# Kernel tuning notes

Measured on AMD Instinct MI355X. Metric: run time of the kernel, lower is better.

Reference implementation:

```python
import jax, jax.numpy as jnp
import numpy as np

N_HEAD, D_K, D_V, D_MODEL, D_O = 8, 64, 64, 512, 512
B, S = 2, 4096

def setup_inputs() -> dict:
    key = jax.random.key(0)
    ks = jax.random.split(key, 11)
    s = 1.0 / np.sqrt(D_MODEL)
    so = 1.0 / np.sqrt(N_HEAD * D_V)
    return {
        'q': jax.random.normal(ks[0], (B, S, D_MODEL), jnp.float32),
        'k': jax.random.normal(ks[1], (B, S, D_MODEL), jnp.float32),
        'v': jax.random.normal(ks[2], (B, S, D_MODEL), jnp.float32),
        'Wq': jax.random.uniform(ks[3], (D_MODEL, N_HEAD * D_K), jnp.float32, -s, s),
        'bq': jax.random.uniform(ks[4], (N_HEAD * D_K,), jnp.float32, -s, s),
        'Wk': jax.random.uniform(ks[5], (D_MODEL, N_HEAD * D_K), jnp.float32, -s, s),
        'bk': jax.random.uniform(ks[6], (N_HEAD * D_K,), jnp.float32, -s, s),
        'Wv': jax.random.uniform(ks[7], (D_MODEL, N_HEAD * D_V), jnp.float32, -s, s),
        'bv': jax.random.uniform(ks[8], (N_HEAD * D_V,), jnp.float32, -s, s),
        'Wo': jax.random.uniform(ks[9], (N_HEAD * D_V, D_O), jnp.float32, -so, so),
        'bo': jax.random.uniform(ks[10], (D_O,), jnp.float32, -so, so),
    }

def reference(q, k, v, Wq, bq, Wk, bk, Wv, bv, Wo, bo):
    b, nq, _ = q.shape
    nk = k.shape[1]
    scale = jnp.asarray(np.power(D_K, 0.5), q.dtype)
    # project and split heads: [b, s, h, d]
    qh = (q @ Wq + bq).reshape(b, nq, N_HEAD, D_K)
    kh = (k @ Wk + bk).reshape(b, nk, N_HEAD, D_K)
    vh = (v @ Wv + bv).reshape(b, nk, N_HEAD, D_V)
    # scaled dot-product attention (full score matrix, as in original)
    scores = jnp.einsum('bqhd,bkhd->bhqk', qh, kh) / scale
    attn = jax.nn.softmax(scores, axis=-1)
    out = jnp.einsum('bhqk,bkhd->bqhd', attn, vh)
    # concat heads (head-major over d_v, matching the original view) and output proj
    out = out.reshape(b, nq, N_HEAD * D_V)
    return out @ Wo + bo
```

## Files before the change

### kernel.cpp

```cpp
#include <hip/hip_runtime.h>
#include <hip/hip_bf16.h>

#define NHEAD 8
#define DK_ 64
#define DM_ 512
#define S_LEN 4096
#define NTOK 8192

typedef __bf16 bf16x8 __attribute__((ext_vector_type(8)));
typedef float f32x4 __attribute__((ext_vector_type(4)));

__device__ __forceinline__ unsigned short f2bf(float f) {
    union { float f; unsigned u; } x; x.f = f;
    unsigned u = x.u;
    u += 0x7FFFu + ((u >> 16) & 1u);
    return (unsigned short)(u >> 16);
}

#if __has_builtin(__builtin_amdgcn_cvt_pk_bf16_f32)
__device__ __forceinline__ unsigned int pkbf(float a, float b) {
    auto r = __builtin_amdgcn_cvt_pk_bf16_f32(a, b);
    unsigned int u; __builtin_memcpy(&u, &r, 4); return u;
}
#else
__device__ __forceinline__ unsigned int pkbf(float a, float b) {
    return (unsigned)f2bf(a) | ((unsigned)f2bf(b) << 16);
}
#endif

#if __has_builtin(__builtin_amdgcn_exp2f)
#define EXP2F(x) __builtin_amdgcn_exp2f(x)
#else
#define EXP2F(x) exp2f(x)
#endif

#define GLOAD_LDS16(gptr, ldsbase) \
    __builtin_amdgcn_global_load_lds((const __attribute__((address_space(1))) unsigned int*)(gptr), \
                                     (__attribute__((address_space(3))) unsigned int*)(ldsbase), 16, 0, 0)

__global__ __launch_bounds__(256) void wtrans(const float* __restrict__ Wq, const float* __restrict__ Wk,
                                              const float* __restrict__ Wv, const float* __restrict__ Wo,
                                              unsigned short* __restrict__ Wt) {
    int z = blockIdx.z;
    const float* W = (z == 0) ? Wq : (z == 1) ? Wk : (z == 2) ? Wv : Wo;
    unsigned short* out = Wt + (size_t)z * DM_ * DM_;
    __shared__ float t[64][65];
    int bn = blockIdx.x * 64, bk = blockIdx.y * 64;
    int tid = threadIdx.x;
    int r0 = tid >> 4, c4 = (tid & 15) * 4;
#pragma unroll
    for (int i = 0; i < 4; i++) {
        int r = r0 + i * 16;
        float4 v = *(const float4*)&W[(size_t)(bk + r) * DM_ + bn + c4];
        t[r][c4] = v.x; t[r][c4 + 1] = v.y; t[r][c4 + 2] = v.z; t[r][c4 + 3] = v.w;
    }
    __syncthreads();
    int n0 = tid >> 4, k4 = (tid & 15) * 4;
#pragma unroll
    for (int i = 0; i < 4; i++) {
        int n = n0 + i * 16;
        ushort4 o;
        o.x = f2bf(t[k4 + 0][n]); o.y = f2bf(t[k4 + 1][n]);
        o.z = f2bf(t[k4 + 2][n]); o.w = f2bf(t[k4 + 3][n]);
        *(ushort4*)&out[(size_t)(bn + n) * DM_ + bk + k4] = o;
    }
}

__global__ __launch_bounds__(256, 3) void qkv_proj(const float* __restrict__ xq, const float* __restrict__ xk,
                                                   const float* __restrict__ xv, const unsigned short* __restrict__ Wt,
                                                   const float* __restrict__ bq, const float* __restrict__ bk,
                                                   const float* __restrict__ bv,
                                                   unsigned short* __restrict__ Qh, unsigned short* __restrict__ Kh,
                                                   unsigned short* __restrict__ VhT) {
    int z = blockIdx.z;
    const float* X = (z == 0) ? xq : (z == 1) ? xk : xv;
    const unsigned short* W = Wt + (size_t)z * DM_ * DM_;
    const float* bias = (z == 0) ? bq : (z == 1) ? bk : bv;
    unsigned short* out = (z == 0) ? Qh : (z == 1) ? Kh : VhT;
    float scale = (z == 0) ? 0.125f * 1.44269504f : 1.0f;

    __shared__ unsigned short As[128 * 40];
    __shared__ unsigned short Bs[128 * 40];
    int tid = threadIdx.x;
    int n0 = blockIdx.x * 128, m0 = blockIdx.y * 128;
    int w = tid >> 6, lane = tid & 63;
    int ln = lane & 15, qd = lane >> 4;
    int mb = (w >> 1) * 64, nb = (w & 1) * 64;

    f32x4 acc[4][4];
#pragma unroll
    for (int i = 0; i < 4; i++)
#pragma unroll
        for (int j = 0; j < 4; j++) { f32x4 zz = {0.f, 0.f, 0.f, 0.f}; acc[i][j] = zz; }

    for (int kk = 0; kk < DM_; kk += 32) {
        __syncthreads();
#pragma unroll
        for (int i = 0; i < 4; i++) {
            int idx = i * 256 + tid;
            int row = idx >> 3, k4 = (idx & 7) * 4;
            float4 v = *(const float4*)&X[(size_t)(m0 + row) * DM_ + kk + k4];
            uint2 o; o.x = pkbf(v.x, v.y); o.y = pkbf(v.z, v.w);
            *(uint2*)&As[row * 40 + k4] = o;
        }
#pragma unroll
        for (int i = 0; i < 2; i++) {
            int idx = i * 256 + tid;
            int row = idx >> 2, k8 = (idx & 3) * 8;
            uint4 v = *(const uint4*)&W[(size_t)(n0 + row) * DM_ + kk + k8];
            *(uint4*)&Bs[row * 40 + k8] = v;
        }
        __syncthreads();
        bf16x8 af[4], bf[4];
#pragma unroll
        for (int mt = 0; mt < 4; mt++) af[mt] = *(const bf16x8*)&As[(mb + mt * 16 + ln) * 40 + qd * 8];
#pragma unroll
        for (int nt = 0; nt < 4; nt++) bf[nt] = *(const bf16x8*)&Bs[(nb + nt * 16 + ln) * 40 + qd * 8];
#pragma unroll
        for (int mt = 0; mt < 4; mt++)
#pragma unroll
            for (int nt = 0; nt < 4; nt++)
                acc[mt][nt] = __builtin_amdgcn_mfma_f32_16x16x32_bf16(af[mt], bf[nt], acc[mt][nt], 0, 0, 0);
    }

    float bvv[4];
#pragma unroll
    for (int nt = 0; nt < 4; nt++) bvv[nt] = bias[n0 + nb + nt * 16 + ln];
#pragma unroll
    for (int mt = 0; mt < 4; mt++) {
        int mrow0 = m0 + mb + mt * 16 + qd * 4;
        int b = mrow0 >> 12, s = mrow0 & 4095;
#pragma unroll
        for (int nt = 0; nt < 4; nt++) {
            int ncol = n0 + nb + nt * 16 + ln;
            int h = ncol >> 6, d = ncol & 63;
            if (z == 2) {
                uint2 o;
                o.x = pkbf((acc[mt][nt][0] + bvv[nt]) * scale, (acc[mt][nt][1] + bvv[nt]) * scale);
                o.y = pkbf((acc[mt][nt][2] + bvv[nt]) * scale, (acc[mt][nt][3] + bvv[nt]) * scale);
                *(uint2*)&out[((size_t)(b * NHEAD + h) * DK_ + d) * S_LEN + s] = o;
            } else {
#pragma unroll
                for (int r = 0; r < 4; r++)
                    out[((size_t)(b * NHEAD + h) * S_LEN + (s + r)) * DK_ + d] =
                        f2bf((acc[mt][nt][r] + bvv[nt]) * scale);
            }
        }
    }
}

__global__ __launch_bounds__(256, 2) void flash_attn(const unsigned short* __restrict__ Qh,
                                                     const unsigned short* __restrict__ Kh,
                                                     const unsigned short* __restrict__ VhT,
                                                     unsigned short* __restrict__ Ao) {
    __shared__ unsigned short Ks[2][64 * 64];
    __shared__ unsigned short Vs[2][64 * 64];
    __shared__ unsigned short Pl[4 * 32 * 72];
    int i = blockIdx.x;
    int bh = (i & 7) + 8 * ((i >> 3) & 1);
    int qb = i >> 4;
    int tid = threadIdx.x;
    int w = tid >> 6, lane = tid & 63;
    int ln = lane & 15, qd = lane >> 4;
    int sw = ln & 7;
    int q0 = qb * 128 + w * 32;
    const unsigned short* Qp = Qh + (size_t)bh * S_LEN * DK_;
    const unsigned short* Kp = Kh + (size_t)bh * S_LEN * DK_;
    const unsigned short* Vp = VhT + (size_t)bh * DK_ * S_LEN;
    unsigned short* pb = &Pl[w * 32 * 72];

    int sr = lane >> 3;
    int sc = (lane & 7) ^ sr;
    const unsigned short* ksrc = Kp + (size_t)(w * 16 + sr) * DK_ + sc * 8;
    const unsigned short* vsrc = Vp + (size_t)(w * 16 + sr) * S_LEN + sc * 8;

    bf16x8 qfA0 = *(const bf16x8*)&Qp[(size_t)(q0 + ln) * DK_ + qd * 8];
    bf16x8 qfA1 = *(const bf16x8*)&Qp[(size_t)(q0 + ln) * DK_ + qd * 8 + 32];
    bf16x8 qfB0 = *(const bf16x8*)&Qp[(size_t)(q0 + 16 + ln) * DK_ + qd * 8];
    bf16x8 qfB1 = *(const bf16x8*)&Qp[(size_t)(q0 + 16 + ln) * DK_ + qd * 8 + 32];

    bf16x8 ones;
#pragma unroll
    for (int j = 0; j < 8; j++) ones[j] = (__bf16)1.0f;

    f32x4 oacc[2][4];
#pragma unroll
    for (int f = 0; f < 2; f++)
#pragma unroll
        for (int j = 0; j < 4; j++) { f32x4 z = {0.f, 0.f, 0.f, 0.f}; oacc[f][j] = z; }
    f32x4 lacc[2];
    { f32x4 z = {0.f, 0.f, 0.f, 0.f}; lacc[0] = z; lacc[1] = z; }

    GLOAD_LDS16(ksrc, &Ks[0][w * 1024]);
    GLOAD_LDS16(ksrc + (size_t)8 * DK_, &Ks[0][w * 1024 + 512]);
    GLOAD_LDS16(vsrc, &Vs[0][w * 1024]);
    GLOAD_LDS16(vsrc + (size_t)8 * S_LEN, &Vs[0][w * 1024 + 512]);

    int p = 0;
    for (int ks = 0; ks < S_LEN; ks += 64, p ^= 1) {
        __syncthreads();
        if (ks + 64 < S_LEN) {
            const unsigned short* kn = ksrc + (size_t)(ks + 64) * DK_;
            const unsigned short* vn = vsrc + (ks + 64);
            GLOAD_LDS16(kn, &Ks[p ^ 1][w * 1024]);
            GLOAD_LDS16(kn + (size_t)8 * DK_, &Ks[p ^ 1][w * 1024 + 512]);
            GLOAD_LDS16(vn, &Vs[p ^ 1][w * 1024]);
            GLOAD_LDS16(vn + (size_t)8 * S_LEN, &Vs[p ^ 1][w * 1024 + 512]);
        }
        const unsigned short* KsT = &Ks[p][0];
        const unsigned short* VsT = &Vs[p][0];

        f32x4 stA[4], stB[4];
#pragma unroll
        for (int t = 0; t < 4; t++) {
            bf16x8 kf0 = *(const bf16x8*)&KsT[(t * 16 + ln) * 64 + (qd ^ sw) * 8];
            bf16x8 kf1 = *(const bf16x8*)&KsT[(t * 16 + ln) * 64 + ((qd + 4) ^ sw) * 8];
            f32x4 zA = {0.f, 0.f, 0.f, 0.f}, zB = {0.f, 0.f, 0.f, 0.f};
            zA = __builtin_amdgcn_mfma_f32_16x16x32_bf16(kf0, qfA0, zA, 0, 0, 0);
            zA = __builtin_amdgcn_mfma_f32_16x16x32_bf16(kf1, qfA1, zA, 0, 0, 0);
            zB = __builtin_amdgcn_mfma_f32_16x16x32_bf16(kf0, qfB0, zB, 0, 0, 0);
            zB = __builtin_amdgcn_mfma_f32_16x16x32_bf16(kf1, qfB1, zB, 0, 0, 0);
            stA[t] = zA; stB[t] = zB;
        }
#pragma unroll
        for (int t = 0; t < 4; t++) {
            uint2 a, b;
            a.x = pkbf(EXP2F(stA[t][0]), EXP2F(stA[t][1]));
            a.y = pkbf(EXP2F(stA[t][2]), EXP2F(stA[t][3]));
            b.x = pkbf(EXP2F(stB[t][0]), EXP2F(stB[t][1]));
            b.y = pkbf(EXP2F(stB[t][2]), EXP2F(stB[t][3]));
            *(uint2*)&pb[ln * 72 + t * 16 + qd * 4] = a;
            *(uint2*)&pb[(16 + ln) * 72 + t * 16 + qd * 4] = b;
        }
        asm volatile("" ::: "memory");
        bf16x8 pA0 = *(const bf16x8*)&pb[ln * 72 + qd * 8];
        bf16x8 pA1 = *(const bf16x8*)&pb[ln * 72 + 32 + qd * 8];
        bf16x8 pB0 = *(const bf16x8*)&pb[(16 + ln) * 72 + qd * 8];
        bf16x8 pB1 = *(const bf16x8*)&pb[(16 + ln) * 72 + 32 + qd * 8];
        lacc[0] = __builtin_amdgcn_mfma_f32_16x16x32_bf16(ones, pA0, lacc[0], 0, 0, 0);
        lacc[0] = __builtin_amdgcn_mfma_f32_16x16x32_bf16(ones, pA1, lacc[0], 0, 0, 0);
        lacc[1] = __builtin_amdgcn_mfma_f32_16x16x32_bf16(ones, pB0, lacc[1], 0, 0, 0);
        lacc[1] = __builtin_amdgcn_mfma_f32_16x16x32_bf16(ones, pB1, lacc[1], 0, 0, 0);
#pragma unroll
        for (int dt = 0; dt < 4; dt++) {
            bf16x8 vf0 = *(const bf16x8*)&VsT[(dt * 16 + ln) * 64 + (qd ^ sw) * 8];
            bf16x8 vf1 = *(const bf16x8*)&VsT[(dt * 16 + ln) * 64 + ((qd + 4) ^ sw) * 8];
            oacc[0][dt] = __builtin_amdgcn_mfma_f32_16x16x32_bf16(vf0, pA0, oacc[0][dt], 0, 0, 0);
            oacc[0][dt] = __builtin_amdgcn_mfma_f32_16x16x32_bf16(vf1, pA1, oacc[0][dt], 0, 0, 0);
            oacc[1][dt] = __builtin_amdgcn_mfma_f32_16x16x32_bf16(vf0, pB0, oacc[1][dt], 0, 0, 0);
            oacc[1][dt] = __builtin_amdgcn_mfma_f32_16x16x32_bf16(vf1, pB1, oacc[1][dt], 0, 0, 0);
        }
    }

    int bb = bh >> 3, hh = bh & 7;
#pragma unroll
    for (int f = 0; f < 2; f++) {
        float inv = 1.0f / lacc[f][0];
        int token = bb * S_LEN + q0 + f * 16 + ln;
#pragma unroll
        for (int dt = 0; dt < 4; dt++) {
            uint2 o;
            o.x = pkbf(oacc[f][dt][0] * inv, oacc[f][dt][1] * inv);
            o.y = pkbf(oacc[f][dt][2] * inv, oacc[f][dt][3] * inv);
            *(uint2*)&Ao[(size_t)token * DM_ + hh * DK_ + dt * 16 + qd * 4] = o;
        }
    }
}

__global__ __launch_bounds__(256) void out_gemm(const unsigned short* __restrict__ A,
                                                const unsigned short* __restrict__ Wt,
                                                const float* __restrict__ bias, float* __restrict__ out) {
    __shared__ unsigned short As[128 * 40];
    __shared__ unsigned short Bs[128 * 40];
    int tid = threadIdx.x;
    int n0 = blockIdx.x * 128, m0 = blockIdx.y * 128;
    int w = tid >> 6, lane = tid & 63;
    int ln = lane & 15, qd = lane >> 4;
    int mb = (w >> 1) * 64, nb = (w & 1) * 64;

    f32x4 acc[4][4];
#pragma unroll
    for (int i = 0; i < 4; i++)
#pragma unroll
        for (int j = 0; j < 4; j++) { f32x4 z = {0.f, 0.f, 0.f, 0.f}; acc[i][j] = z; }

    for (int kk = 0; kk < DM_; kk += 32) {
        __syncthreads();
#pragma unroll
        for (int i = 0; i < 2; i++) {
            int idx = i * 256 + tid;
            int row = idx >> 2, k8 = (idx & 3) * 8;
            uint4 va = *(const uint4*)&A[(size_t)(m0 + row) * DM_ + kk + k8];
            *(uint4*)&As[row * 40 + k8] = va;
            uint4 vb = *(const uint4*)&Wt[(size_t)(n0 + row) * DM_ + kk + k8];
            *(uint4*)&Bs[row * 40 + k8] = vb;
        }
        __syncthreads();
        bf16x8 af[4], bf[4];
#pragma unroll
        for (int mt = 0; mt < 4; mt++) af[mt] = *(const bf16x8*)&As[(mb + mt * 16 + ln) * 40 + qd * 8];
#pragma unroll
        for (int nt = 0; nt < 4; nt++) bf[nt] = *(const bf16x8*)&Bs[(nb + nt * 16 + ln) * 40 + qd * 8];
#pragma unroll
        for (int mt = 0; mt < 4; mt++)
#pragma unroll
            for (int nt = 0; nt < 4; nt++)
                acc[mt][nt] = __builtin_amdgcn_mfma_f32_16x16x32_bf16(af[mt], bf[nt], acc[mt][nt], 0, 0, 0);
    }

    float bv[4];
#pragma unroll
    for (int nt = 0; nt < 4; nt++) bv[nt] = bias[n0 + nb + nt * 16 + ln];
#pragma unroll
    for (int mt = 0; mt < 4; mt++) {
        int mrow0 = m0 + mb + mt * 16 + qd * 4;
#pragma unroll
        for (int nt = 0; nt < 4; nt++) {
            int ncol = n0 + nb + nt * 16 + ln;
#pragma unroll
            for (int r = 0; r < 4; r++)
                out[(size_t)(mrow0 + r) * DM_ + ncol] = acc[mt][nt][r] + bv[nt];
        }
    }
}

extern "C" void kernel_launch(void* const* d_in, const int* in_sizes, int n_in,
                              void* d_out, int out_size, void* d_ws, size_t ws_size,
                              hipStream_t stream) {
    const float* q  = (const float*)d_in[0];
    const float* k  = (const float*)d_in[1];
    const float* v  = (const float*)d_in[2];
    const float* Wq = (const float*)d_in[3];
    const float* bq = (const float*)d_in[4];
    const float* Wk = (const float*)d_in[5];
    const float* bk = (const float*)d_in[6];
    const float* Wv = (const float*)d_in[7];
    const float* bv = (const float*)d_in[8];
    const float* Wo = (const float*)d_in[9];
    const float* bo = (const float*)d_in[10];
    float* out = (float*)d_out;

    unsigned short* Wt  = (unsigned short*)d_ws;
    unsigned short* Qh  = Wt + (size_t)4 * DM_ * DM_;
    unsigned short* Kh  = Qh + (size_t)NTOK * DM_;
    unsigned short* VhT = Kh + (size_t)NTOK * DM_;
    unsigned short* Ao  = VhT + (size_t)NTOK * DM_;

    wtrans<<<dim3(8, 8, 4), 256, 0, stream>>>(Wq, Wk, Wv, Wo, Wt);
    qkv_proj<<<dim3(4, 64, 3), 256, 0, stream>>>(q, k, v, Wt, bq, bk, bv, Qh, Kh, VhT);
    flash_attn<<<dim3(512), 256, 0, stream>>>(Qh, Kh, VhT, Ao);
    out_gemm<<<dim3(4, 64), 256, 0, stream>>>(Ao, Wt + (size_t)3 * DM_ * DM_, bo, out);
}
```

Measured before the change: 251.5 us.

## Pre-convert inputs to bf16 and enlarge flash attention query tile per wave

Adds a separate pass that converts the fp32 q/k/v inputs to bf16 into workspace, so the projection GEMM can load bf16 tiles directly instead of converting inside its loop. That path is taken only when the workspace is large enough. The attention kernel now gives each wave 64 queries instead of 32 and splits each key tile into two halves. This reuses every K/V fragment across four query subtiles, with 256 blocks at one block per SM. The costs are higher register pressure, fewer resident waves, and an extra kernel launch plus a round trip through global memory for the conversion.

```diff
diff --git a/kernel.cpp b/kernel.cpp
--- a/kernel.cpp
+++ b/kernel.cpp
@@ -37,6 +37,16 @@
 #define GLOAD_LDS16(gptr, ldsbase) \
     __builtin_amdgcn_global_load_lds((const __attribute__((address_space(1))) unsigned int*)(gptr), \
                                      (__attribute__((address_space(3))) unsigned int*)(ldsbase), 16, 0, 0)
+
+__global__ __launch_bounds__(256) void xcvt(const float* __restrict__ q, const float* __restrict__ k,
+                                            const float* __restrict__ v, unsigned short* __restrict__ Xbf) {
+    int z = blockIdx.y;
+    const float* X = (z == 0) ? q : (z == 1) ? k : v;
+    size_t off = (size_t)blockIdx.x * 1024 + threadIdx.x * 4;
+    float4 val = *(const float4*)&X[off];
+    uint2 o; o.x = pkbf(val.x, val.y); o.y = pkbf(val.z, val.w);
+    *(uint2*)&Xbf[(size_t)z * NTOK * DM_ + off] = o;
+}
 
 __global__ __launch_bounds__(256) void wtrans(const float* __restrict__ Wq, const float* __restrict__ Wk,
                                               const float* __restrict__ Wv, const float* __restrict__ Wo,
@@ -64,6 +74,88 @@
         o.z = f2bf(t[k4 + 2][n]); o.w = f2bf(t[k4 + 3][n]);
         *(ushort4*)&out[(size_t)(bn + n) * DM_ + bk + k4] = o;
     }
+}
+
+__device__ __forceinline__ void proj_epilogue(int z, f32x4 (&acc)[4][4], const float* bias,
+                                              unsigned short* out, float scale,
+                                              int m0, int n0, int mb, int nb, int ln, int qd) {
+    float bvv[4];
+#pragma unroll
+    for (int nt = 0; nt < 4; nt++) bvv[nt] = bias[n0 + nb + nt * 16 + ln];
+#pragma unroll
+    for (int mt = 0; mt < 4; mt++) {
+        int mrow0 = m0 + mb + mt * 16 + qd * 4;
+        int b = mrow0 >> 12, s = mrow0 & 4095;
+#pragma unroll
+        for (int nt = 0; nt < 4; nt++) {
+            int ncol = n0 + nb + nt * 16 + ln;
+            int h = ncol >> 6, d = ncol & 63;
+            if (z == 2) {
+                uint2 o;
+                o.x = pkbf((acc[mt][nt][0] + bvv[nt]) * scale, (acc[mt][nt][1] + bvv[nt]) * scale);
+                o.y = pkbf((acc[mt][nt][2] + bvv[nt]) * scale, (acc[mt][nt][3] + bvv[nt]) * scale);
+                *(uint2*)&out[((size_t)(b * NHEAD + h) * DK_ + d) * S_LEN + s] = o;
+            } else {
+#pragma unroll
+                for (int r = 0; r < 4; r++)
+                    out[((size_t)(b * NHEAD + h) * S_LEN + (s + r)) * DK_ + d] =
+                        f2bf((acc[mt][nt][r] + bvv[nt]) * scale);
+            }
+        }
+    }
+}
+
+__global__ __launch_bounds__(256, 3) void qkv_bf(const unsigned short* __restrict__ Xbf,
+                                                 const unsigned short* __restrict__ Wt,
+                                                 const float* __restrict__ bq, const float* __restrict__ bk,
+                                                 const float* __restrict__ bv,
+                                                 unsigned short* __restrict__ Qh, unsigned short* __restrict__ Kh,
+                                                 unsigned short* __restrict__ VhT) {
+    int z = blockIdx.z;
+    const unsigned short* X = Xbf + (size_t)z * NTOK * DM_;
+    const unsigned short* W = Wt + (size_t)z * DM_ * DM_;
+    const float* bias = (z == 0) ? bq : (z == 1) ? bk : bv;
+    unsigned short* out = (z == 0) ? Qh : (z == 1) ? Kh : VhT;
+    float scale = (z == 0) ? 0.125f * 1.44269504f : 1.0f;
+
+    __shared__ unsigned short As[128 * 40];
+    __shared__ unsigned short Bs[128 * 40];
+    int tid = threadIdx.x;
+    int n0 = blockIdx.x * 128, m0 = blockIdx.y * 128;
+    int w = tid >> 6, lane = tid & 63;
+    int ln = lane & 15, qd = lane >> 4;
+    int mb = (w >> 1) * 64, nb = (w & 1) * 64;
+
+    f32x4 acc[4][4];
+#pragma unroll
+    for (int i = 0; i < 4; i++)
+#pragma unroll
+        for (int j = 0; j < 4; j++) { f32x4 zz = {0.f, 0.f, 0.f, 0.f}; acc[i][j] = zz; }
+
+    for (int kk = 0; kk < DM_; kk += 32) {
+        __syncthreads();
+#pragma unroll
+        for (int i = 0; i < 2; i++) {
+            int idx = i * 256 + tid;
+            int row = idx >> 2, k8 = (idx & 3) * 8;
+            uint4 va = *(const uint4*)&X[(size_t)(m0 + row) * DM_ + kk + k8];
+            *(uint4*)&As[row * 40 + k8] = va;
+            uint4 vb = *(const uint4*)&W[(size_t)(n0 + row) * DM_ + kk + k8];
+            *(uint4*)&Bs[row * 40 + k8] = vb;
+        }
+        __syncthreads();
+        bf16x8 af[4], bf[4];
+#pragma unroll
+        for (int mt = 0; mt < 4; mt++) af[mt] = *(const bf16x8*)&As[(mb + mt * 16 + ln) * 40 + qd * 8];
+#pragma unroll
+        for (int nt = 0; nt < 4; nt++) bf[nt] = *(const bf16x8*)&Bs[(nb + nt * 16 + ln) * 40 + qd * 8];
+#pragma unroll
+        for (int mt = 0; mt < 4; mt++)
+#pragma unroll
+            for (int nt = 0; nt < 4; nt++)
+                acc[mt][nt] = __builtin_amdgcn_mfma_f32_16x16x32_bf16(af[mt], bf[nt], acc[mt][nt], 0, 0, 0);
+    }
+    proj_epilogue(z, acc, bias, out, scale, m0, n0, mb, nb, ln, qd);
 }
 
 __global__ __launch_bounds__(256, 3) void qkv_proj(const float* __restrict__ xq, const float* __restrict__ xk,
@@ -122,40 +214,16 @@
             for (int nt = 0; nt < 4; nt++)
                 acc[mt][nt] = __builtin_amdgcn_mfma_f32_16x16x32_bf16(af[mt], bf[nt], acc[mt][nt], 0, 0, 0);
     }
-
-    float bvv[4];
-#pragma unroll
-    for (int nt = 0; nt < 4; nt++) bvv[nt] = bias[n0 + nb + nt * 16 + ln];
-#pragma unroll
-    for (int mt = 0; mt < 4; mt++) {
-        int mrow0 = m0 + mb + mt * 16 + qd * 4;
-        int b = mrow0 >> 12, s = mrow0 & 4095;
-#pragma unroll
-        for (int nt = 0; nt < 4; nt++) {
-            int ncol = n0 + nb + nt * 16 + ln;
-            int h = ncol >> 6, d = ncol & 63;
-            if (z == 2) {
-                uint2 o;
-                o.x = pkbf((acc[mt][nt][0] + bvv[nt]) * scale, (acc[mt][nt][1] + bvv[nt]) * scale);
-                o.y = pkbf((acc[mt][nt][2] + bvv[nt]) * scale, (acc[mt][nt][3] + bvv[nt]) * scale);
-                *(uint2*)&out[((size_t)(b * NHEAD + h) * DK_ + d) * S_LEN + s] = o;
-            } else {
-#pragma unroll
-                for (int r = 0; r < 4; r++)
-                    out[((size_t)(b * NHEAD + h) * S_LEN + (s + r)) * DK_ + d] =
-                        f2bf((acc[mt][nt][r] + bvv[nt]) * scale);
-            }
-        }
-    }
-}
-
-__global__ __launch_bounds__(256, 2) void flash_attn(const unsigned short* __restrict__ Qh,
+    proj_epilogue(z, acc, bias, out, scale, m0, n0, mb, nb, ln, qd);
+}
+
+__global__ __launch_bounds__(256, 1) void flash_attn(const unsigned short* __restrict__ Qh,
                                                      const unsigned short* __restrict__ Kh,
                                                      const unsigned short* __restrict__ VhT,
                                                      unsigned short* __restrict__ Ao) {
     __shared__ unsigned short Ks[2][64 * 64];
     __shared__ unsigned short Vs[2][64 * 64];
-    __shared__ unsigned short Pl[4 * 32 * 72];
+    __shared__ unsigned short Pl[4][64 * 36];
     int i = blockIdx.x;
     int bh = (i & 7) + 8 * ((i >> 3) & 1);
     int qb = i >> 4;
@@ -163,33 +231,37 @@
     int w = tid >> 6, lane = tid & 63;
     int ln = lane & 15, qd = lane >> 4;
     int sw = ln & 7;
-    int q0 = qb * 128 + w * 32;
+    int q0 = qb * 256 + w * 64;
     const unsigned short* Qp = Qh + (size_t)bh * S_LEN * DK_;
     const unsigned short* Kp = Kh + (size_t)bh * S_LEN * DK_;
     const unsigned short* Vp = VhT + (size_t)bh * DK_ * S_LEN;
-    unsigned short* pb = &Pl[w * 32 * 72];
+    unsigned short* pb = &Pl[w][0];
 
     int sr = lane >> 3;
     int sc = (lane & 7) ^ sr;
     const unsigned short* ksrc = Kp + (size_t)(w * 16 + sr) * DK_ + sc * 8;
     const unsigned short* vsrc = Vp + (size_t)(w * 16 + sr) * S_LEN + sc * 8;
 
-    bf16x8 qfA0 = *(const bf16x8*)&Qp[(size_t)(q0 + ln) * DK_ + qd * 8];
-    bf16x8 qfA1 = *(const bf16x8*)&Qp[(size_t)(q0 + ln) * DK_ + qd * 8 + 32];
-    bf16x8 qfB0 = *(const bf16x8*)&Qp[(size_t)(q0 + 16 + ln) * DK_ + qd * 8];
-    bf16x8 qfB1 = *(const bf16x8*)&Qp[(size_t)(q0 + 16 + ln) * DK_ + qd * 8 + 32];
+    bf16x8 qf[4][2];
+#pragma unroll
+    for (int f = 0; f < 4; f++) {
+        const unsigned short* qr = &Qp[(size_t)(q0 + f * 16 + ln) * DK_ + qd * 8];
+        qf[f][0] = *(const bf16x8*)qr;
+        qf[f][1] = *(const bf16x8*)(qr + 32);
+    }
 
     bf16x8 ones;
 #pragma unroll
     for (int j = 0; j < 8; j++) ones[j] = (__bf16)1.0f;
 
-    f32x4 oacc[2][4];
-#pragma unroll
-    for (int f = 0; f < 2; f++)
+    f32x4 oacc[4][4];
+#pragma unroll
+    for (int f = 0; f < 4; f++)
 #pragma unroll
         for (int j = 0; j < 4; j++) { f32x4 z = {0.f, 0.f, 0.f, 0.f}; oacc[f][j] = z; }
-    f32x4 lacc[2];
-    { f32x4 z = {0.f, 0.f, 0.f, 0.f}; lacc[0] = z; lacc[1] = z; }
+    f32x4 lacc[4];
+#pragma unroll
+    for (int f = 0; f < 4; f++) { f32x4 z = {0.f, 0.f, 0.f, 0.f}; lacc[f] = z; }
 
     GLOAD_LDS16(ksrc, &Ks[0][w * 1024]);
     GLOAD_LDS16(ksrc + (size_t)8 * DK_, &Ks[0][w * 1024 + 512]);
@@ -210,51 +282,53 @@
         const unsigned short* KsT = &Ks[p][0];
         const unsigned short* VsT = &Vs[p][0];
 
-        f32x4 stA[4], stB[4];
-#pragma unroll
-        for (int t = 0; t < 4; t++) {
-            bf16x8 kf0 = *(const bf16x8*)&KsT[(t * 16 + ln) * 64 + (qd ^ sw) * 8];
-            bf16x8 kf1 = *(const bf16x8*)&KsT[(t * 16 + ln) * 64 + ((qd + 4) ^ sw) * 8];
-            f32x4 zA = {0.f, 0.f, 0.f, 0.f}, zB = {0.f, 0.f, 0.f, 0.f};
-            zA = __builtin_amdgcn_mfma_f32_16x16x32_bf16(kf0, qfA0, zA, 0, 0, 0);
-            zA = __builtin_amdgcn_mfma_f32_16x16x32_bf16(kf1, qfA1, zA, 0, 0, 0);
-            zB = __builtin_amdgcn_mfma_f32_16x16x32_bf16(kf0, qfB0, zB, 0, 0, 0);
-            zB = __builtin_amdgcn_mfma_f32_16x16x32_bf16(kf1, qfB1, zB, 0, 0, 0);
-            stA[t] = zA; stB[t] = zB;
-        }
-#pragma unroll
-        for (int t = 0; t < 4; t++) {
-            uint2 a, b;
-            a.x = pkbf(EXP2F(stA[t][0]), EXP2F(stA[t][1]));
-            a.y = pkbf(EXP2F(stA[t][2]), EXP2F(stA[t][3]));
-            b.x = pkbf(EXP2F(stB[t][0]), EXP2F(stB[t][1]));
-            b.y = pkbf(EXP2F(stB[t][2]), EXP2F(stB[t][3]));
-            *(uint2*)&pb[ln * 72 + t * 16 + qd * 4] = a;
-            *(uint2*)&pb[(16 + ln) * 72 + t * 16 + qd * 4] = b;
-        }
-        asm volatile("" ::: "memory");
-        bf16x8 pA0 = *(const bf16x8*)&pb[ln * 72 + qd * 8];
-        bf16x8 pA1 = *(const bf16x8*)&pb[ln * 72 + 32 + qd * 8];
-        bf16x8 pB0 = *(const bf16x8*)&pb[(16 + ln) * 72 + qd * 8];
-        bf16x8 pB1 = *(const bf16x8*)&pb[(16 + ln) * 72 + 32 + qd * 8];
-        lacc[0] = __builtin_amdgcn_mfma_f32_16x16x32_bf16(ones, pA0, lacc[0], 0, 0, 0);
-        lacc[0] = __builtin_amdgcn_mfma_f32_16x16x32_bf16(ones, pA1, lacc[0], 0, 0, 0);
-        lacc[1] = __builtin_amdgcn_mfma_f32_16x16x32_bf16(ones, pB0, lacc[1], 0, 0, 0);
-        lacc[1] = __builtin_amdgcn_mfma_f32_16x16x32_bf16(ones, pB1, lacc[1], 0, 0, 0);
-#pragma unroll
-        for (int dt = 0; dt < 4; dt++) {
-            bf16x8 vf0 = *(const bf16x8*)&VsT[(dt * 16 + ln) * 64 + (qd ^ sw) * 8];
-            bf16x8 vf1 = *(const bf16x8*)&VsT[(dt * 16 + ln) * 64 + ((qd + 4) ^ sw) * 8];
-            oacc[0][dt] = __builtin_amdgcn_mfma_f32_16x16x32_bf16(vf0, pA0, oacc[0][dt], 0, 0, 0);
-            oacc[0][dt] = __builtin_amdgcn_mfma_f32_16x16x32_bf16(vf1, pA1, oacc[0][dt], 0, 0, 0);
-            oacc[1][dt] = __builtin_amdgcn_mfma_f32_16x16x32_bf16(vf0, pB0, oacc[1][dt], 0, 0, 0);
-            oacc[1][dt] = __builtin_amdgcn_mfma_f32_16x16x32_bf16(vf1, pB1, oacc[1][dt], 0, 0, 0);
+#pragma unroll
+        for (int h = 0; h < 2; h++) {
+            f32x4 st[4][2];
+#pragma unroll
+            for (int f = 0; f < 4; f++)
+#pragma unroll
+                for (int t = 0; t < 2; t++) { f32x4 z = {0.f, 0.f, 0.f, 0.f}; st[f][t] = z; }
+#pragma unroll
+            for (int t = 0; t < 2; t++) {
+                int kt = h * 2 + t;
+                bf16x8 kf0 = *(const bf16x8*)&KsT[(kt * 16 + ln) * 64 + (qd ^ sw) * 8];
+                bf16x8 kf1 = *(const bf16x8*)&KsT[(kt * 16 + ln) * 64 + ((qd + 4) ^ sw) * 8];
+#pragma unroll
+                for (int f = 0; f < 4; f++) {
+                    st[f][t] = __builtin_amdgcn_mfma_f32_16x16x32_bf16(kf0, qf[f][0], st[f][t], 0, 0, 0);
+                    st[f][t] = __builtin_amdgcn_mfma_f32_16x16x32_bf16(kf1, qf[f][1], st[f][t], 0, 0, 0);
+                }
+            }
+#pragma unroll
+            for (int f = 0; f < 4; f++)
+#pragma unroll
+                for (int t = 0; t < 2; t++) {
+                    uint2 a;
+                    a.x = pkbf(EXP2F(st[f][t][0]), EXP2F(st[f][t][1]));
+                    a.y = pkbf(EXP2F(st[f][t][2]), EXP2F(st[f][t][3]));
+                    *(uint2*)&pb[(f * 16 + ln) * 36 + t * 16 + qd * 4] = a;
+                }
+            asm volatile("" ::: "memory");
+            bf16x8 pf[4];
+#pragma unroll
+            for (int f = 0; f < 4; f++) pf[f] = *(const bf16x8*)&pb[(f * 16 + ln) * 36 + qd * 8];
+#pragma unroll
+            for (int f = 0; f < 4; f++)
+                lacc[f] = __builtin_amdgcn_mfma_f32_16x16x32_bf16(ones, pf[f], lacc[f], 0, 0, 0);
+#pragma unroll
+            for (int dt = 0; dt < 4; dt++) {
+                bf16x8 vf = *(const bf16x8*)&VsT[(dt * 16 + ln) * 64 + ((h * 4 + qd) ^ sw) * 8];
+#pragma unroll
+                for (int f = 0; f < 4; f++)
+                    oacc[f][dt] = __builtin_amdgcn_mfma_f32_16x16x32_bf16(vf, pf[f], oacc[f][dt], 0, 0, 0);
+            }
         }
     }
 
     int bb = bh >> 3, hh = bh & 7;
 #pragma unroll
-    for (int f = 0; f < 2; f++) {
+    for (int f = 0; f < 4; f++) {
         float inv = 1.0f / lacc[f][0];
         int token = bb * S_LEN + q0 + f * 16 + ln;
 #pragma unroll
@@ -344,10 +418,19 @@
     unsigned short* Qh  = Wt + (size_t)4 * DM_ * DM_;
     unsigned short* Kh  = Qh + (size_t)NTOK * DM_;
     unsigned short* VhT = Kh + (size_t)NTOK * DM_;
-    unsigned short* Ao  = VhT + (size_t)NTOK * DM_;
+    unsigned short* tail = VhT + (size_t)NTOK * DM_;
+
+    size_t need_bf = ((size_t)4 * DM_ * DM_ + (size_t)6 * NTOK * DM_) * 2;
 
     wtrans<<<dim3(8, 8, 4), 256, 0, stream>>>(Wq, Wk, Wv, Wo, Wt);
-    qkv_proj<<<dim3(4, 64, 3), 256, 0, stream>>>(q, k, v, Wt, bq, bk, bv, Qh, Kh, VhT);
-    flash_attn<<<dim3(512), 256, 0, stream>>>(Qh, Kh, VhT, Ao);
+    unsigned short* Ao = tail;
+    if (ws_size >= need_bf) {
+        unsigned short* Xbf = tail;
+        xcvt<<<dim3(4096, 3), 256, 0, stream>>>(q, k, v, Xbf);
+        qkv_bf<<<dim3(4, 64, 3), 256, 0, stream>>>(Xbf, Wt, bq, bk, bv, Qh, Kh, VhT);
+    } else {
+        qkv_proj<<<dim3(4, 64, 3), 256, 0, stream>>>(q, k, v, Wt, bq, bk, bv, Qh, Kh, VhT);
+    }
+    flash_attn<<<dim3(256), 256, 0, stream>>>(Qh, Kh, VhT, Ao);
     out_gemm<<<dim3(4, 64), 256, 0, stream>>>(Ao, Wt + (size_t)3 * DM_ * DM_, bo, out);
 }
```

Result: slower. 333.9 us (+32.8%).
